# Optimization experiments

Measured on AMD Instinct MI355X. Metric: run time of the kernel, lower is better.

## Reference

```python
import jax, jax.numpy as jnp
import numpy as np

B, S, E, H, D = 4, 2048, 1024, 16, 64  # batch, seq, embed, heads, head_dim


def setup_inputs() -> dict:
    key = jax.random.key(0)
    k1, k2, k3 = jax.random.split(key, 3)
    x = jax.random.normal(k1, (B, S, E), dtype=jnp.float32)
    qkv_w = jax.random.normal(k2, (E, H, 3 * D), dtype=jnp.float32) * (1.0 / np.sqrt(E))
    qkv_b = jnp.zeros((H, 3 * D), dtype=jnp.float32)
    out_w = jax.random.normal(k3, (H, D, E), dtype=jnp.float32) * (1.0 / np.sqrt(H * D))
    out_b = jnp.zeros((E,), dtype=jnp.float32)
    return {"x": x, "qkv_w": qkv_w, "qkv_b": qkv_b, "out_w": out_w, "out_b": out_b}


def _large_negative_number(dtype):
    return jnp.asarray(-0.7 * jnp.finfo(dtype).max, dtype=dtype)


def reference(x, qkv_w, qkv_b, out_w, out_b):
    # qkv projection: LinearGeneral(E -> (H, 3D))
    qkv = jnp.einsum('bse,ehd->bshd', x, qkv_w) + qkv_b  # [B,S,H,3D]
    q, k, v = jnp.split(qkv, 3, axis=-1)  # each [B,S,H,D]
    logits = jnp.einsum('bqhd,bkhd->bhqk', q, k)  # [B,H,S,S]
    logits = logits / jnp.sqrt(jnp.asarray(q.shape[-1], logits.dtype))
    mask = jnp.tril(jnp.ones((q.shape[1], q.shape[1]), dtype=jnp.bool_))
    logits = jnp.where(mask, logits, _large_negative_number(logits.dtype))
    probs = jax.nn.softmax(logits, axis=-1)
    attn = jnp.einsum('bhqk,bkhd->bqhd', probs, v)  # [B,S,H,D]
    # output projection: LinearGeneral((H, D) -> E)
    return jnp.einsum('bqhd,hde->bqe', attn, out_w) + out_b
```

## Files before the change

kernel.cpp:

```cpp
#include <hip/hip_runtime.h>

typedef unsigned int u32;
typedef _Float16 f16;
typedef _Float16 f16x8 __attribute__((ext_vector_type(8)));
typedef _Float16 f16x4 __attribute__((ext_vector_type(4)));
typedef float f32x4 __attribute__((ext_vector_type(4)));
typedef _Float16 __attribute__((address_space(3))) lf16;

#define LOG2E 1.4426950408889634f

__device__ __forceinline__ void gl_lds16(const void* g, void* l) {
  __builtin_amdgcn_global_load_lds(
      (const __attribute__((address_space(1))) u32*)g,
      (__attribute__((address_space(3))) u32*)l, 16, 0, 0);
}

__device__ __forceinline__ f32x4 mfma16(f16x8 a, f16x8 b, f32x4 c) {
  return __builtin_amdgcn_mfma_f32_16x16x32_f16(a, b, c, 0, 0, 0);
}

__device__ __forceinline__ f16x8 ldsr(const f16* p) {
  f16x8 r;
  asm volatile("ds_read_b128 %0, %1" : "=v"(r) : "v"((const lf16*)p));
  return r;
}

__global__ void k_cvt(const float* __restrict__ in, f16* __restrict__ out, int n4) {
  int stride = gridDim.x * blockDim.x;
  for (int i = blockIdx.x * blockDim.x + threadIdx.x; i < n4; i += stride) {
    f32x4 v = *(const f32x4*)(in + (size_t)i * 4);
    f16x4 o;
    o[0] = (f16)v[0]; o[1] = (f16)v[1]; o[2] = (f16)v[2]; o[3] = (f16)v[3];
    *(f16x4*)(out + (size_t)i * 4) = o;
  }
}

__global__ void k_tconv(const float* __restrict__ in, f16* __restrict__ out, int R, int C) {
  __shared__ f16 tile[32][33];
  int c0 = blockIdx.x * 32, r0 = blockIdx.y * 32;
  int tx = threadIdx.x, ty = threadIdx.y;
#pragma unroll
  for (int i = ty; i < 32; i += 8)
    tile[i][tx] = (f16)in[(size_t)(r0 + i) * C + c0 + tx];
  __syncthreads();
#pragma unroll
  for (int i = ty; i < 32; i += 8)
    out[(size_t)(c0 + i) * R + r0 + tx] = tile[tx][i];
}

__device__ __forceinline__ void gemm_fatA(
    const f16* __restrict__ A, const f16* __restrict__ Bt,
    int bm, int bn, f16* SM, int w, int lane, f32x4 (&acc)[8][4]) {
  constexpr int KT = 32;
  const int g = lane >> 4, rl = lane & 15;
  const int l4 = lane >> 2, ls = lane & 3;
  const int sslot = ls ^ ((l4 >> 1) & 3);

  const f16* aS = A + (size_t)(bm + w * 32 + l4) * 1024 + sslot * 8;
  const f16* bS = Bt + (size_t)(bn + w * 16 + l4) * 1024 + sslot * 8;
  f16* aD = SM + w * 1024;
  f16* bD = SM + 4096 + w * 512;

#define ASTG0(b, kt) do { \
    gl_lds16(aS + (kt) * 32,          aD + (b) * 12288); \
    gl_lds16(aS + 16384 + (kt) * 32,  aD + (b) * 12288 + 512); \
    gl_lds16(bS + (kt) * 32,          bD + (b) * 12288); } while (0)
#define ASTG1(b, kt) do { \
    gl_lds16(bS + 65536 + (kt) * 32,  bD + (b) * 12288 + 2048); \
    gl_lds16(bS + 131072 + (kt) * 32, bD + (b) * 12288 + 4096); \
    gl_lds16(bS + 196608 + (kt) * 32, bD + (b) * 12288 + 6144); } while (0)

  ASTG0(0, 0); ASTG1(0, 0);
  ASTG0(1, 1); ASTG1(1, 1);
  asm volatile("s_waitcnt vmcnt(6)" ::: "memory");
  __builtin_amdgcn_s_barrier();

  const int ro = rl * 32 + ((g ^ ((rl >> 1) & 3)) * 8);

  int c = 0, cs = 2;
#pragma unroll 1
  for (int kt = 0; kt < KT; ++kt) {
    const f16* SMc = SM + c * 12288;
    const bool stg = (kt + 2 < KT);
    f16x8 bf[4], af[4];

    {
#pragma unroll
      for (int j = 0; j < 4; ++j)
        bf[j] = ldsr(SMc + 4096 + w * 2048 + j * 512 + ro);
#pragma unroll
      for (int mi = 0; mi < 4; ++mi)
        af[mi] = ldsr(SMc + mi * 512 + ro);
      if (stg) ASTG0(cs, kt + 2);
      __builtin_amdgcn_s_barrier();
      asm volatile("s_waitcnt lgkmcnt(0)");
      __builtin_amdgcn_sched_barrier(0);
      __builtin_amdgcn_s_setprio(1);
#pragma unroll
      for (int mi = 0; mi < 4; ++mi)
#pragma unroll
        for (int j = 0; j < 4; ++j)
          acc[mi][j] = mfma16(af[mi], bf[j], acc[mi][j]);
      __builtin_amdgcn_s_setprio(0);
      __builtin_amdgcn_sched_barrier(0);
      __builtin_amdgcn_s_barrier();
    }
    {
#pragma unroll
      for (int mi = 0; mi < 4; ++mi)
        af[mi] = ldsr(SMc + (4 + mi) * 512 + ro);
      if (stg) ASTG1(cs, kt + 2);
      __builtin_amdgcn_s_barrier();
      asm volatile("s_waitcnt lgkmcnt(0)");
      __builtin_amdgcn_sched_barrier(0);
      __builtin_amdgcn_s_setprio(1);
#pragma unroll
      for (int mi = 0; mi < 4; ++mi)
#pragma unroll
        for (int j = 0; j < 4; ++j)
          acc[4 + mi][j] = mfma16(af[mi], bf[j], acc[4 + mi][j]);
      __builtin_amdgcn_s_setprio(0);
      __builtin_amdgcn_sched_barrier(0);
      if (kt + 2 < KT)      { asm volatile("s_waitcnt vmcnt(6)" ::: "memory"); }
      else if (kt + 1 < KT) { asm volatile("s_waitcnt vmcnt(0)" ::: "memory"); }
      __builtin_amdgcn_s_barrier();
      __builtin_amdgcn_sched_barrier(0);
    }
    c = (c == 2) ? 0 : c + 1;
    cs = (cs == 2) ? 0 : cs + 1;
  }
#undef ASTG0
#undef ASTG1
}

__device__ __forceinline__ void gemm_fatC(
    const f16* __restrict__ A, const f16* __restrict__ Bt,
    int bm, int bn, f16* SM, int w, int lane, f32x4 (&acc)[8][4]) {
  constexpr int KT = 32;
  const int g = lane >> 4, rl = lane & 15;
  const int l4 = lane >> 2, ls = lane & 3;
  const int sslot = ls ^ ((l4 >> 1) & 3);

  const f16* aS = A + (size_t)(bm + w * 32 + l4) * 1024 + sslot * 8;
  const f16* bS = Bt + (size_t)(bn + w * 16 + l4) * 1024 + sslot * 8;
  f16* aD = SM + w * 1024;
  f16* bD = SM + 4096 + w * 512;

#define CSTG0(b, kt) do { \
    gl_lds16(aS + (kt) * 32,          aD + (b) * 12288); \
    gl_lds16(aS + 16384 + (kt) * 32,  aD + (b) * 12288 + 512); \
    gl_lds16(bS + (kt) * 32,          bD + (b) * 12288); } while (0)
#define CSTG1(b, kt) do { \
    gl_lds16(bS + 65536 + (kt) * 32,  bD + (b) * 12288 + 2048); \
    gl_lds16(bS + 131072 + (kt) * 32, bD + (b) * 12288 + 4096); \
    gl_lds16(bS + 196608 + (kt) * 32, bD + (b) * 12288 + 6144); } while (0)

  CSTG0(0, 0); CSTG1(0, 0);
  CSTG0(1, 1); CSTG1(1, 1);
  asm volatile("s_waitcnt vmcnt(6)" ::: "memory");
  __builtin_amdgcn_s_barrier();

  const int ro = rl * 32 + ((g ^ ((rl >> 1) & 3)) * 8);

  int c = 0, cs = 2;
#pragma unroll 1
  for (int kt = 0; kt < KT; ++kt) {
    const f16* SMc = SM + c * 12288;
    const bool stg = (kt + 2 < KT);
    f16x8 bf[4], af[4];
    {
#pragma unroll
      for (int j = 0; j < 4; ++j)
        bf[j] = *(const f16x8*)(SMc + 4096 + w * 2048 + j * 512 + ro);
#pragma unroll
      for (int mi = 0; mi < 4; ++mi)
        af[mi] = *(const f16x8*)(SMc + mi * 512 + ro);
      if (stg) CSTG0(cs, kt + 2);
      __builtin_amdgcn_s_barrier();
      asm volatile("s_waitcnt lgkmcnt(0)" ::: "memory");
      __builtin_amdgcn_sched_barrier(0);
      __builtin_amdgcn_s_setprio(1);
#pragma unroll
      for (int mi = 0; mi < 4; ++mi)
#pragma unroll
        for (int j = 0; j < 4; ++j)
          acc[mi][j] = mfma16(af[mi], bf[j], acc[mi][j]);
      __builtin_amdgcn_s_setprio(0);
      __builtin_amdgcn_sched_barrier(0);
      __builtin_amdgcn_s_barrier();
    }
    {
#pragma unroll
      for (int mi = 0; mi < 4; ++mi)
        af[mi] = *(const f16x8*)(SMc + (4 + mi) * 512 + ro);
      if (stg) CSTG1(cs, kt + 2);
      __builtin_amdgcn_s_barrier();
      asm volatile("s_waitcnt lgkmcnt(0)" ::: "memory");
      __builtin_amdgcn_sched_barrier(0);
      __builtin_amdgcn_s_setprio(1);
#pragma unroll
      for (int mi = 0; mi < 4; ++mi)
#pragma unroll
        for (int j = 0; j < 4; ++j)
          acc[4 + mi][j] = mfma16(af[mi], bf[j], acc[4 + mi][j]);
      __builtin_amdgcn_s_setprio(0);
      __builtin_amdgcn_sched_barrier(0);
      if (kt + 2 < KT)      { asm volatile("s_waitcnt vmcnt(6)" ::: "memory"); }
      else if (kt + 1 < KT) { asm volatile("s_waitcnt vmcnt(0)" ::: "memory"); }
      __builtin_amdgcn_s_barrier();
      __builtin_amdgcn_sched_barrier(0);
    }
    c = (c == 2) ? 0 : c + 1;
    cs = (cs == 2) ? 0 : cs + 1;
  }
#undef CSTG0
#undef CSTG1
}

__global__ __launch_bounds__(256, 2) void k_gemm_qkv4(
    const f16* __restrict__ A, const f16* __restrict__ Bt,
    const float* __restrict__ bias,
    f16* __restrict__ qo, f16* __restrict__ ko2, f16* __restrict__ vto) {
  __shared__ __align__(16) f16 SM[36864];
  const int lin0 = blockIdx.y * 12 + blockIdx.x;
  const int lin = (lin0 & 7) * 96 + (lin0 >> 3);
  const int bn = (lin % 12) * 256, bm = (lin / 12) * 128;
  const int t = threadIdx.x, lane = t & 63, w = t >> 6;
  const int g = lane >> 4, rl = lane & 15;

  f32x4 acc[8][4] = {};
  gemm_fatA(A, Bt, bm, bn, SM, w, lane, acc);

#pragma unroll
  for (int mi = 0; mi < 8; ++mi)
#pragma unroll
    for (int j = 0; j < 4; ++j)
#pragma unroll
      for (int r = 0; r < 4; ++r) {
        int m = bm + mi * 16 + g * 4 + r;
        int n = bn + w * 64 + j * 16 + rl;
        float v = acc[mi][j][r] + bias[n];
        int b = m >> 11, s = m & 2047;
        int h = n / 192, rem = n - h * 192;
        int tsel = rem >> 6, d = rem & 63;
        size_t bh = (size_t)(b * 16 + h);
        if (tsel == 0)      qo[(bh * 2048 + s) * 64 + d] = (f16)(v * (0.125f * LOG2E));
        else if (tsel == 1) ko2[(bh * 2048 + s) * 64 + d] = (f16)v;
        else                vto[(bh * 64 + d) * 2048 + s] = (f16)v;
      }
}

__global__ __launch_bounds__(256, 2) void k_gemm_out4(
    const f16* __restrict__ A, const f16* __restrict__ Bt,
    const float* __restrict__ bias, float* __restrict__ out) {
  __shared__ __align__(16) f16 SM[36864];
  const int lin0 = blockIdx.y * 4 + blockIdx.x;
  const int lin = (lin0 & 7) * 32 + (lin0 >> 3);
  const int bn = (lin % 4) * 256, bm = (lin / 4) * 128;
  const int t = threadIdx.x, lane = t & 63, w = t >> 6;
  const int g = lane >> 4, rl = lane & 15;

  f32x4 acc[8][4] = {};
  gemm_fatC(A, Bt, bm, bn, SM, w, lane, acc);

#pragma unroll
  for (int mi = 0; mi < 8; ++mi)
#pragma unroll
    for (int j = 0; j < 4; ++j)
#pragma unroll
      for (int r = 0; r < 4; ++r) {
        int m = bm + mi * 16 + g * 4 + r;
        int n = bn + w * 64 + j * 16 + rl;
        out[(size_t)m * 1024 + n] = acc[mi][j][r] + bias[n];
      }
}

__global__ __launch_bounds__(256, 2) void k_attn4(
    const f16* __restrict__ q, const f16* __restrict__ kgl,
    const f16* __restrict__ vt, f16* __restrict__ o) {
  constexpr int S = 2048;
  __shared__ __align__(16) f16 Ks[2][64 * 64];
  __shared__ __align__(16) f16 Vs[2][64 * 64];
  __shared__ __align__(16) f16 Ps[4][16 * 64];

  const int blk = blockIdx.x;
  const int bh = (blk & 7) * 8 + ((blk >> 3) & 7);
  const int p = blk >> 6;

  const int t = threadIdx.x, lane = t & 63, w = t >> 6;
  const int g = lane >> 4, rl = lane & 15;

  const f16* kb = kgl + (size_t)bh * S * 64;
  const f16* vb = vt + (size_t)bh * 64 * S;
  const int srow = lane >> 3;
  const int sslot = (lane & 7) ^ srow;
  const int h = bh & 15;

  auto STAGE = [&](int bufi, int kt) {
#pragma unroll
    for (int i = 0; i < 2; ++i) {
      const int r0 = w * 16 + i * 8;
      gl_lds16(kb + (size_t)(kt * 64 + r0 + srow) * 64 + sslot * 8, &Ks[bufi][r0 * 64]);
      gl_lds16(vb + (size_t)(r0 + srow) * S + kt * 64 + sslot * 8, &Vs[bufi][r0 * 64]);
    }
  };

#pragma unroll 1
  for (int half = 0; half < 2; ++half) {
    const int qb = half ? p : 15 - p;
    const f16* qp = q + ((size_t)bh * S + qb * 128) * 64;

    f16x8 qf[2][2];
#pragma unroll
    for (int sub = 0; sub < 2; ++sub)
#pragma unroll
      for (int ks = 0; ks < 2; ++ks)
        qf[sub][ks] = *(const f16x8*)(qp + (size_t)(w * 32 + sub * 16 + rl) * 64 + ks * 32 + g * 8);

    f32x4 oacc[2][4] = {};
    float lrow[2] = {0.f, 0.f};

    const int nkt = 2 * qb + 2;
    const int qmaxw = qb * 128 + w * 32 + 31;

    STAGE(0, 0);
    __syncthreads();
    int buf = 0;

    for (int kt = 0; kt < nkt; ++kt) {
      if (kt + 1 < nkt) STAGE(buf ^ 1, kt + 1);

      if (kt * 64 <= qmaxw) {
        const f16* Kb = &Ks[buf][0];
        const f16* Vb = &Vs[buf][0];
#pragma unroll
        for (int sub = 0; sub < 2; ++sub) {
          const int qsub = qb * 128 + w * 32 + sub * 16;
          if (kt * 64 > qsub + 15) continue;

          f32x4 sT[4] = {};
#pragma unroll
          for (int j = 0; j < 4; ++j)
#pragma unroll
            for (int ks = 0; ks < 2; ++ks) {
              int row = j * 16 + rl;
              f16x8 kf = *(const f16x8*)(Kb + row * 64 + (((ks * 4 + g) ^ (rl & 7)) * 8));
              sT[j] = mfma16(kf, qf[sub][ks], sT[j]);
            }

          if (kt * 64 + 63 > qsub) {
#pragma unroll
            for (int j = 0; j < 4; ++j)
#pragma unroll
              for (int r = 0; r < 4; ++r)
                if (kt * 64 + j * 16 + g * 4 + r > qsub + rl) sT[j][r] = -1e30f;
          }

          float ps = 0.f;
#pragma unroll
          for (int j = 0; j < 4; ++j) {
            f16x4 pb;
#pragma unroll
            for (int r = 0; r < 4; ++r) {
              float pp = exp2f(sT[j][r]);
              ps += pp;
              pb[r] = (f16)pp;
            }
            *(f16x4*)(&Ps[w][0] + rl * 64 + (((j * 2 + (g >> 1)) ^ (rl & 7)) * 8) + (g & 1) * 4) = pb;
          }
          lrow[sub] += ps;

          asm volatile("s_waitcnt lgkmcnt(0)" ::: "memory");
          __builtin_amdgcn_sched_barrier(0);

          f16x8 pf[2];
#pragma unroll
          for (int ks = 0; ks < 2; ++ks)
            pf[ks] = *(const f16x8*)(&Ps[w][0] + rl * 64 + (((ks * 4 + g) ^ (rl & 7)) * 8));

#pragma unroll
          for (int dj = 0; dj < 4; ++dj)
#pragma unroll
            for (int ks = 0; ks < 2; ++ks) {
              int vrow = dj * 16 + rl;
              f16x8 vf = *(const f16x8*)(Vb + vrow * 64 + (((ks * 4 + g) ^ (rl & 7)) * 8));
              oacc[sub][dj] = mfma16(pf[ks], vf, oacc[sub][dj]);
            }
        }
      }
      __syncthreads();
      buf ^= 1;
    }

    float rinv[2];
#pragma unroll
    for (int sub = 0; sub < 2; ++sub) {
      float s_ = lrow[sub];
      s_ += __shfl_xor(s_, 16, 64);
      s_ += __shfl_xor(s_, 32, 64);
      rinv[sub] = 1.0f / s_;
    }

    const size_t rowb = (size_t)(bh >> 4) * 2048 + qb * 128 + w * 32;
#pragma unroll
    for (int sub = 0; sub < 2; ++sub)
#pragma unroll
      for (int r = 0; r < 4; ++r) {
        float ri = __shfl(rinv[sub], g * 4 + r, 64);
#pragma unroll
        for (int dj = 0; dj < 4; ++dj)
          o[(rowb + sub * 16 + g * 4 + r) * 1024 + h * 64 + dj * 16 + rl] =
              (f16)(oacc[sub][dj][r] * ri);
      }
  }
}

extern "C" void kernel_launch(void* const* d_in, const int* in_sizes, int n_in,
                              void* d_out, int out_size, void* d_ws, size_t ws_size,
                              hipStream_t stream) {
  (void)in_sizes; (void)n_in; (void)out_size; (void)ws_size;
  const float* x    = (const float*)d_in[0];
  const float* wqkv = (const float*)d_in[1];
  const float* bqkv = (const float*)d_in[2];
  const float* wo   = (const float*)d_in[3];
  const float* bo   = (const float*)d_in[4];
  float* out = (float*)d_out;
  char* ws = (char*)d_ws;

  f16* xb    = (f16*)(ws + 0);
  f16* wqkvt = (f16*)(ws + 16777216);
  f16* wot   = (f16*)(ws + 23068672);
  f16* qws   = (f16*)(ws + 25165824);
  f16* kws   = (f16*)(ws + 41943040);
  f16* vtws  = (f16*)(ws + 58720256);
  f16* attnb = xb;

  k_cvt<<<2048, 256, 0, stream>>>(x, xb, 8388608 / 4);
  k_tconv<<<dim3(96, 32), dim3(32, 8), 0, stream>>>(wqkv, wqkvt, 1024, 3072);
  k_tconv<<<dim3(32, 32), dim3(32, 8), 0, stream>>>(wo, wot, 1024, 1024);
  k_gemm_qkv4<<<dim3(12, 64), 256, 0, stream>>>(xb, wqkvt, bqkv, qws, kws, vtws);
  k_attn4<<<512, 256, 0, stream>>>(qws, kws, vtws, attnb);
  k_gemm_out4<<<dim3(4, 64), 256, 0, stream>>>(attnb, wot, bo, out);
}
```

Before: 199.3 us.

## Split attention into one q-block per workgroup with interleaved causal ordering

The attention kernel no longer has each workgroup process two paired q-blocks in sequence. It now launches 1024 workgroups, one per 128-row q-block, in a causal-aware ordering that interleaves heavy and light blocks, and raises launch bounds to 4 waves per SIMD for more occupancy. Both q sub-tiles' QK^T MFMAs are also computed together from each K fragment load, which halves K LDS reads. The costs are more register pressure under the tighter occupancy bound, and losing the paired load balancing if scheduling order does not hold.

```diff
diff --git a/kernel.cpp b/kernel.cpp
--- a/kernel.cpp
+++ b/kernel.cpp
@@ -242,11 +242,11 @@
         float v = acc[mi][j][r] + bias[n];
         int b = m >> 11, s = m & 2047;
         int h = n / 192, rem = n - h * 192;
-        int tsel = rem >> 6, d = rem & 63;
+        int tsel = rem >> 6, dd = rem & 63;
         size_t bh = (size_t)(b * 16 + h);
-        if (tsel == 0)      qo[(bh * 2048 + s) * 64 + d] = (f16)(v * (0.125f * LOG2E));
-        else if (tsel == 1) ko2[(bh * 2048 + s) * 64 + d] = (f16)v;
-        else                vto[(bh * 64 + d) * 2048 + s] = (f16)v;
+        if (tsel == 0)      qo[(bh * 2048 + s) * 64 + dd] = (f16)(v * (0.125f * LOG2E));
+        else if (tsel == 1) ko2[(bh * 2048 + s) * 64 + dd] = (f16)v;
+        else                vto[(bh * 64 + dd) * 2048 + s] = (f16)v;
       }
 }
 
@@ -275,7 +275,7 @@
       }
 }
 
-__global__ __launch_bounds__(256, 2) void k_attn4(
+__global__ __launch_bounds__(256, 4) void k_attn5(
     const f16* __restrict__ q, const f16* __restrict__ kgl,
     const f16* __restrict__ vt, f16* __restrict__ o) {
   constexpr int S = 2048;
@@ -283,18 +283,34 @@
   __shared__ __align__(16) f16 Vs[2][64 * 64];
   __shared__ __align__(16) f16 Ps[4][16 * 64];
 
-  const int blk = blockIdx.x;
-  const int bh = (blk & 7) * 8 + ((blk >> 3) & 7);
-  const int p = blk >> 6;
+  const int d = blockIdx.x;
+  const int bh = (d & 7) * 8 + ((d >> 3) & 7);
+  const int v_ = d >> 6, g2 = v_ >> 2, r2 = v_ & 3;
+  const int qb = (g2 == 0) ? 15 - r2 : (g2 == 1) ? r2 : (g2 == 2) ? 11 - r2 : 4 + r2;
 
   const int t = threadIdx.x, lane = t & 63, w = t >> 6;
   const int g = lane >> 4, rl = lane & 15;
 
+  const f16* qp = q + ((size_t)bh * S + qb * 128) * 64;
   const f16* kb = kgl + (size_t)bh * S * 64;
   const f16* vb = vt + (size_t)bh * 64 * S;
+
+  f16x8 qf[2][2];
+#pragma unroll
+  for (int sub = 0; sub < 2; ++sub)
+#pragma unroll
+    for (int ks = 0; ks < 2; ++ks)
+      qf[sub][ks] = *(const f16x8*)(qp + (size_t)(w * 32 + sub * 16 + rl) * 64 + ks * 32 + g * 8);
+
+  f32x4 oacc[2][4] = {};
+  float lrow[2] = {0.f, 0.f};
+
   const int srow = lane >> 3;
   const int sslot = (lane & 7) ^ srow;
-  const int h = bh & 15;
+
+  const int nkt = 2 * qb + 2;
+  const int qsub0 = qb * 128 + w * 32;
+  const int qmaxw = qsub0 + 31;
 
   auto STAGE = [&](int bufi, int kt) {
 #pragma unroll
@@ -305,114 +321,102 @@
     }
   };
 
-#pragma unroll 1
-  for (int half = 0; half < 2; ++half) {
-    const int qb = half ? p : 15 - p;
-    const f16* qp = q + ((size_t)bh * S + qb * 128) * 64;
-
-    f16x8 qf[2][2];
-#pragma unroll
-    for (int sub = 0; sub < 2; ++sub)
-#pragma unroll
-      for (int ks = 0; ks < 2; ++ks)
-        qf[sub][ks] = *(const f16x8*)(qp + (size_t)(w * 32 + sub * 16 + rl) * 64 + ks * 32 + g * 8);
-
-    f32x4 oacc[2][4] = {};
-    float lrow[2] = {0.f, 0.f};
-
-    const int nkt = 2 * qb + 2;
-    const int qmaxw = qb * 128 + w * 32 + 31;
-
-    STAGE(0, 0);
-    __syncthreads();
-    int buf = 0;
-
-    for (int kt = 0; kt < nkt; ++kt) {
-      if (kt + 1 < nkt) STAGE(buf ^ 1, kt + 1);
-
-      if (kt * 64 <= qmaxw) {
-        const f16* Kb = &Ks[buf][0];
-        const f16* Vb = &Vs[buf][0];
+  STAGE(0, 0);
+  __syncthreads();
+  int buf = 0;
+
+  for (int kt = 0; kt < nkt; ++kt) {
+    if (kt + 1 < nkt) STAGE(buf ^ 1, kt + 1);
+
+    if (kt * 64 <= qmaxw) {
+      const f16* Kb = &Ks[buf][0];
+      const f16* Vb = &Vs[buf][0];
+
+      f32x4 sT[2][4] = {};
+#pragma unroll
+      for (int j = 0; j < 4; ++j)
+#pragma unroll
+        for (int ks = 0; ks < 2; ++ks) {
+          int row = j * 16 + rl;
+          f16x8 kf = *(const f16x8*)(Kb + row * 64 + (((ks * 4 + g) ^ (rl & 7)) * 8));
+          sT[0][j] = mfma16(kf, qf[0][ks], sT[0][j]);
+          sT[1][j] = mfma16(kf, qf[1][ks], sT[1][j]);
+        }
+
+      if (kt * 64 + 63 > qsub0) {
 #pragma unroll
         for (int sub = 0; sub < 2; ++sub) {
-          const int qsub = qb * 128 + w * 32 + sub * 16;
-          if (kt * 64 > qsub + 15) continue;
-
-          f32x4 sT[4] = {};
+          const int qs = qsub0 + sub * 16;
 #pragma unroll
           for (int j = 0; j < 4; ++j)
 #pragma unroll
-            for (int ks = 0; ks < 2; ++ks) {
-              int row = j * 16 + rl;
-              f16x8 kf = *(const f16x8*)(Kb + row * 64 + (((ks * 4 + g) ^ (rl & 7)) * 8));
-              sT[j] = mfma16(kf, qf[sub][ks], sT[j]);
-            }
-
-          if (kt * 64 + 63 > qsub) {
-#pragma unroll
-            for (int j = 0; j < 4; ++j)
-#pragma unroll
-              for (int r = 0; r < 4; ++r)
-                if (kt * 64 + j * 16 + g * 4 + r > qsub + rl) sT[j][r] = -1e30f;
-          }
-
-          float ps = 0.f;
-#pragma unroll
-          for (int j = 0; j < 4; ++j) {
-            f16x4 pb;
-#pragma unroll
-            for (int r = 0; r < 4; ++r) {
-              float pp = exp2f(sT[j][r]);
-              ps += pp;
-              pb[r] = (f16)pp;
-            }
-            *(f16x4*)(&Ps[w][0] + rl * 64 + (((j * 2 + (g >> 1)) ^ (rl & 7)) * 8) + (g & 1) * 4) = pb;
-          }
-          lrow[sub] += ps;
-
-          asm volatile("s_waitcnt lgkmcnt(0)" ::: "memory");
-          __builtin_amdgcn_sched_barrier(0);
-
-          f16x8 pf[2];
-#pragma unroll
-          for (int ks = 0; ks < 2; ++ks)
-            pf[ks] = *(const f16x8*)(&Ps[w][0] + rl * 64 + (((ks * 4 + g) ^ (rl & 7)) * 8));
-
-#pragma unroll
-          for (int dj = 0; dj < 4; ++dj)
-#pragma unroll
-            for (int ks = 0; ks < 2; ++ks) {
-              int vrow = dj * 16 + rl;
-              f16x8 vf = *(const f16x8*)(Vb + vrow * 64 + (((ks * 4 + g) ^ (rl & 7)) * 8));
-              oacc[sub][dj] = mfma16(pf[ks], vf, oacc[sub][dj]);
-            }
+            for (int r = 0; r < 4; ++r)
+              if (kt * 64 + j * 16 + g * 4 + r > qs + rl) sT[sub][j][r] = -1e30f;
         }
       }
-      __syncthreads();
-      buf ^= 1;
-    }
-
-    float rinv[2];
-#pragma unroll
-    for (int sub = 0; sub < 2; ++sub) {
-      float s_ = lrow[sub];
-      s_ += __shfl_xor(s_, 16, 64);
-      s_ += __shfl_xor(s_, 32, 64);
-      rinv[sub] = 1.0f / s_;
-    }
-
-    const size_t rowb = (size_t)(bh >> 4) * 2048 + qb * 128 + w * 32;
-#pragma unroll
-    for (int sub = 0; sub < 2; ++sub)
-#pragma unroll
-      for (int r = 0; r < 4; ++r) {
-        float ri = __shfl(rinv[sub], g * 4 + r, 64);
+
+#pragma unroll
+      for (int sub = 0; sub < 2; ++sub) {
+        const int qsub = qsub0 + sub * 16;
+        if (kt * 64 > qsub + 15) continue;
+
+        float ps = 0.f;
+#pragma unroll
+        for (int j = 0; j < 4; ++j) {
+          f16x4 pb;
+#pragma unroll
+          for (int r = 0; r < 4; ++r) {
+            float pp = exp2f(sT[sub][j][r]);
+            ps += pp;
+            pb[r] = (f16)pp;
+          }
+          *(f16x4*)(&Ps[w][0] + rl * 64 + (((j * 2 + (g >> 1)) ^ (rl & 7)) * 8) + (g & 1) * 4) = pb;
+        }
+        lrow[sub] += ps;
+
+        asm volatile("s_waitcnt lgkmcnt(0)" ::: "memory");
+        __builtin_amdgcn_sched_barrier(0);
+
+        f16x8 pf[2];
+#pragma unroll
+        for (int ks = 0; ks < 2; ++ks)
+          pf[ks] = *(const f16x8*)(&Ps[w][0] + rl * 64 + (((ks * 4 + g) ^ (rl & 7)) * 8));
+
 #pragma unroll
         for (int dj = 0; dj < 4; ++dj)
-          o[(rowb + sub * 16 + g * 4 + r) * 1024 + h * 64 + dj * 16 + rl] =
-              (f16)(oacc[sub][dj][r] * ri);
+#pragma unroll
+          for (int ks = 0; ks < 2; ++ks) {
+            int vrow = dj * 16 + rl;
+            f16x8 vf = *(const f16x8*)(Vb + vrow * 64 + (((ks * 4 + g) ^ (rl & 7)) * 8));
+            oacc[sub][dj] = mfma16(pf[ks], vf, oacc[sub][dj]);
+          }
       }
+    }
+    __syncthreads();
+    buf ^= 1;
   }
+
+  float rinv[2];
+#pragma unroll
+  for (int sub = 0; sub < 2; ++sub) {
+    float s_ = lrow[sub];
+    s_ += __shfl_xor(s_, 16, 64);
+    s_ += __shfl_xor(s_, 32, 64);
+    rinv[sub] = 1.0f / s_;
+  }
+
+  const int h = bh & 15;
+  const size_t rowb = (size_t)(bh >> 4) * 2048 + qb * 128 + w * 32;
+#pragma unroll
+  for (int sub = 0; sub < 2; ++sub)
+#pragma unroll
+    for (int r = 0; r < 4; ++r) {
+      float ri = __shfl(rinv[sub], g * 4 + r, 64);
+#pragma unroll
+      for (int dj = 0; dj < 4; ++dj)
+        o[(rowb + sub * 16 + g * 4 + r) * 1024 + h * 64 + dj * 16 + rl] =
+            (f16)(oacc[sub][dj][r] * ri);
+    }
 }
 
 extern "C" void kernel_launch(void* const* d_in, const int* in_sizes, int n_in,
@@ -439,6 +443,6 @@
   k_tconv<<<dim3(96, 32), dim3(32, 8), 0, stream>>>(wqkv, wqkvt, 1024, 3072);
   k_tconv<<<dim3(32, 32), dim3(32, 8), 0, stream>>>(wo, wot, 1024, 1024);
   k_gemm_qkv4<<<dim3(12, 64), 256, 0, stream>>>(xb, wqkvt, bqkv, qws, kws, vtws);
-  k_attn4<<<512, 256, 0, stream>>>(qws, kws, vtws, attnb);
+  k_attn5<<<1024, 256, 0, stream>>>(qws, kws, vtws, attnb);
   k_gemm_out4<<<dim3(4, 64), 256, 0, stream>>>(attnb, wot, bo, out);
 }
```

After: 187.9 us. -5.7%, faster.
